# Performance work log

Measured on AMD Instinct MI355X. Metric: run time of the kernel, lower is better.

## Reference

```python
import jax, jax.numpy as jnp
import numpy as np

CUTOFF = 5.0   # radius cutoff r
N_BASIS = 20   # radial Bessel basis size
P = 9          # polynomial cutoff degree
BOX = 40.0     # box edge length (Angstrom) for atom positions
N_ATOMS = 2048


def setup_inputs() -> dict:
    key = jax.random.key(0)
    # atoms uniformly distributed in a cubic box -> realistic sparse radius graph
    pos = jax.random.uniform(key, (N_ATOMS, 3), dtype=jnp.float32) * BOX
    return {"pos": pos}


def reference(pos):
    """EdgeEmbedding.forward (cell=None, batch=None), dense-masked jit form.

    Returns:
      dist_edge: [N, N, n_basis]  envelope(d/r) * bessel(d/r), zero outside radius/diagonal
      dir_edge:  [N, N, 3]        unit displacement vectors, zero outside radius/diagonal
      mask:      [N, N] bool      valid-edge mask (replaces dynamic edge_index)
    """
    r, p, n_basis = CUTOFF, P, N_BASIS
    n = pos.shape[0]
    disp = pos[:, None, :] - pos[None, :, :]          # [N, N, 3], disp[i,j] = pos[i]-pos[j]
    dist = jnp.sqrt(jnp.sum(disp * disp, axis=-1))    # [N, N]
    eye = jnp.eye(n, dtype=bool)
    mask = (dist < r) & (~eye)                        # RadiusGraph: i != j and |d| < r

    safe_dist = jnp.where(mask, dist, 1.0)            # avoid 0-div on diagonal / masked
    dir_edge = jnp.where(mask[..., None], disp / safe_dist[..., None], 0.0)  # ScaledNorm dir
    x = safe_dist / r                                 # ScaledNorm scaled distance

    # PolynomialCutoff: 1 - .5(p+1)(p+2)x^p + p(p+2)x^(p+1) - .5 p(p+1)x^(p+2)
    xp = x ** p
    env = 1.0 - 0.5 * (p + 1) * (p + 2) * xp + p * (p + 2) * xp * x - 0.5 * p * (p + 1) * xp * x * x

    # RadialBesselLayer: sin(k*pi*x)/x for k = 1..n_basis
    freqs = jnp.arange(1, n_basis + 1, dtype=pos.dtype) * jnp.pi  # [n_basis]
    bessel = jnp.sin(freqs * x[..., None]) / x[..., None]         # [N, N, n_basis]

    dist_edge = jnp.where(mask[..., None], env[..., None] * bessel, 0.0)
    return (dist_edge, dir_edge, mask)
```

## Files before the change

### kernel.cpp

```cpp
#include <hip/hip_runtime.h>
#include <math.h>


#define NATOMS 2048
#define NBASIS 20
#define RCUT   5.0f

__global__ __launch_bounds__(256) void edge_scan_kernel(
    const float* __restrict__ pos, float* __restrict__ out)
{
    const int t = threadIdx.x;
    const int i = blockIdx.x >> 3;
    const int j = ((blockIdx.x & 7) << 8) | t;

    const float xi = pos[3 * i + 0], yi = pos[3 * i + 1], zi = pos[3 * i + 2];
    const float xj = pos[3 * j + 0], yj = pos[3 * j + 1], zj = pos[3 * j + 2];
    const float dx = xi - xj, dy = yi - yj, dz = zi - zj;
    float d2;
    {
#pragma clang fp contract(off)
        d2 = (dx * dx + dy * dy) + dz * dz;
    }
    const float dist = sqrtf(d2);
    if (!((dist < RCUT) && (i != j))) return;

    const float x  = dist * (1.0f / RCUT);
    const float x2 = x * x, x4 = x2 * x2, x8 = x4 * x4, x9 = x8 * x;
    const float env = 1.0f - 55.0f * x9 + 99.0f * x9 * x - 45.0f * x9 * x2;
    const float scale = env / x;

    const float theta = 3.14159265358979323846f * x;
    const float s1 = sinf(theta);
    const float twoc = 2.0f * cosf(theta);
    float vals[NBASIS];
    float pm2 = 0.0f, pm1 = s1;
    vals[0] = scale * s1;
#pragma unroll
    for (int k = 1; k < NBASIS; ++k) {
        const float sk = twoc * pm1 - pm2;
        vals[k] = scale * sk;
        pm2 = pm1; pm1 = sk;
    }

    const long long pair = (long long)i * NATOMS + j;
    float4* __restrict__ deq = (float4*)(out + pair * NBASIS);
#pragma unroll
    for (int q = 0; q < 5; ++q)
        deq[q] = make_float4(vals[4 * q + 0], vals[4 * q + 1], vals[4 * q + 2], vals[4 * q + 3]);

    const float inv = 1.0f / dist;
    float* __restrict__ dir = out + (long long)NATOMS * NATOMS * NBASIS + pair * 3;
    dir[0] = dx * inv; dir[1] = dy * inv; dir[2] = dz * inv;
    out[(long long)NATOMS * NATOMS * (NBASIS + 3) + pair] = 1.0f;
}

extern "C" void kernel_launch(void* const* d_in, const int* in_sizes, int n_in,
                              void* d_out, int out_size, void* d_ws, size_t ws_size,
                              hipStream_t stream) {
    const float* pos = (const float*)d_in[0];
    float* out = (float*)d_out;
    hipMemsetAsync(out, 0, (size_t)out_size * sizeof(float), stream);
    edge_scan_kernel<<<dim3(NATOMS * 8), dim3(256), 0, stream>>>(pos, out);
}
```

Measured before the change: 406.3 us.

## Fuse zero-fill into single grid-stride kernel writing every output element once

Drops the separate memset plus sparse scattered writes. One persistent grid-stride kernel now writes every float4 of the basis, direction and mask regions directly, computing zeros for masked pairs. Each output byte is written once and coalesced instead of twice. The cost is recomputing the pair distance per float4 chunk, and doing sin evaluations per chunk rather than once per pair.

```diff
diff --git a/kernel.cpp b/kernel.cpp
--- a/kernel.cpp
+++ b/kernel.cpp
@@ -2,56 +2,117 @@
 #include <math.h>
 
 
-#define NATOMS 2048
-#define NBASIS 20
-#define RCUT   5.0f
+#define NATOMS  2048
+#define NBASIS  20
+#define RCUT    5.0f
+#define NTHREADS (4096 * 256)
 
-__global__ __launch_bounds__(256) void edge_scan_kernel(
+__global__ __launch_bounds__(256) void edge_embed_fused(
     const float* __restrict__ pos, float* __restrict__ out)
 {
-    const int t = threadIdx.x;
-    const int i = blockIdx.x >> 3;
-    const int j = ((blockIdx.x & 7) << 8) | t;
+    const unsigned tid = blockIdx.x * 256u + threadIdx.x;
 
-    const float xi = pos[3 * i + 0], yi = pos[3 * i + 1], zi = pos[3 * i + 2];
-    const float xj = pos[3 * j + 0], yj = pos[3 * j + 1], zj = pos[3 * j + 2];
-    const float dx = xi - xj, dy = yi - yj, dz = zi - zj;
-    float d2;
     {
+        float4* __restrict__ deq = (float4*)out;
+        const unsigned nqA = (unsigned)NATOMS * NATOMS * 5u;
+#pragma unroll 1
+        for (unsigned g = tid; g < nqA; g += NTHREADS) {
+            const unsigned pair = __umulhi(g, 0xCCCCCCCDu) >> 2;
+            const unsigned q    = g - pair * 5u;
+            const unsigned i    = pair >> 11, j = pair & 2047u;
+            const float xi = pos[3*i], yi = pos[3*i+1], zi = pos[3*i+2];
+            const float xj = pos[3*j], yj = pos[3*j+1], zj = pos[3*j+2];
+            const float dx = xi - xj, dy = yi - yj, dz = zi - zj;
+            float d2;
+            {
 #pragma clang fp contract(off)
-        d2 = (dx * dx + dy * dy) + dz * dz;
-    }
-    const float dist = sqrtf(d2);
-    if (!((dist < RCUT) && (i != j))) return;
-
-    const float x  = dist * (1.0f / RCUT);
-    const float x2 = x * x, x4 = x2 * x2, x8 = x4 * x4, x9 = x8 * x;
-    const float env = 1.0f - 55.0f * x9 + 99.0f * x9 * x - 45.0f * x9 * x2;
-    const float scale = env / x;
-
-    const float theta = 3.14159265358979323846f * x;
-    const float s1 = sinf(theta);
-    const float twoc = 2.0f * cosf(theta);
-    float vals[NBASIS];
-    float pm2 = 0.0f, pm1 = s1;
-    vals[0] = scale * s1;
-#pragma unroll
-    for (int k = 1; k < NBASIS; ++k) {
-        const float sk = twoc * pm1 - pm2;
-        vals[k] = scale * sk;
-        pm2 = pm1; pm1 = sk;
+                d2 = (dx * dx + dy * dy) + dz * dz;
+            }
+            const float dist = sqrtf(d2);
+            float4 v = make_float4(0.f, 0.f, 0.f, 0.f);
+            if ((dist < RCUT) && (i != j)) {
+                const float x  = dist * (1.0f / RCUT);
+                const float x2 = x * x, x4 = x2 * x2, x8 = x4 * x4, x9 = x8 * x;
+                const float env = 1.0f - 55.0f * x9 + 99.0f * x9 * x - 45.0f * x9 * x2;
+                const float scale = env / x;
+                const float theta = 3.14159265358979323846f * x;
+                const float k0 = (float)(4u * q + 1u);
+                const float s0 = sinf(k0 * theta);
+                const float s1 = sinf(k0 * theta + theta);
+                const float twoc = 2.0f * cosf(theta);
+                const float s2 = twoc * s1 - s0;
+                const float s3 = twoc * s2 - s1;
+                v = make_float4(scale * s0, scale * s1, scale * s2, scale * s3);
+            }
+            deq[g] = v;
+        }
     }
 
-    const long long pair = (long long)i * NATOMS + j;
-    float4* __restrict__ deq = (float4*)(out + pair * NBASIS);
+    {
+        float4* __restrict__ dirq = (float4*)(out + (size_t)NATOMS * NATOMS * NBASIS);
+        const unsigned nqB = (unsigned)NATOMS * NATOMS * 3u / 4u;
+#pragma unroll 1
+        for (unsigned g = tid; g < nqB; g += NTHREADS) {
+            const unsigned f0 = 4u * g;
+            const unsigned p0 = __umulhi(f0, 0xAAAAAAABu) >> 1;
+            const unsigned c0 = f0 - p0 * 3u;
+            float o[6];
 #pragma unroll
-    for (int q = 0; q < 5; ++q)
-        deq[q] = make_float4(vals[4 * q + 0], vals[4 * q + 1], vals[4 * q + 2], vals[4 * q + 3]);
+            for (int s = 0; s < 2; ++s) {
+                const unsigned p = p0 + (unsigned)s;
+                const unsigned i = (p >> 11) & 2047u, j = p & 2047u;
+                const float dx = pos[3*i]   - pos[3*j];
+                const float dy = pos[3*i+1] - pos[3*j+1];
+                const float dz = pos[3*i+2] - pos[3*j+2];
+                float d2;
+                {
+#pragma clang fp contract(off)
+                    d2 = (dx * dx + dy * dy) + dz * dz;
+                }
+                const float dist = sqrtf(d2);
+                const bool m = (dist < RCUT) && (i != j);
+                const float inv = m ? (1.0f / dist) : 0.0f;
+                o[3*s]   = dx * inv;
+                o[3*s+1] = dy * inv;
+                o[3*s+2] = dz * inv;
+            }
+            float4 v;
+            float* ve = (float*)&v;
+#pragma unroll
+            for (int e = 0; e < 4; ++e) {
+                const unsigned ce = c0 + (unsigned)e;
+                ve[e] = (ce == 0) ? o[0] : (ce == 1) ? o[1] : (ce == 2) ? o[2]
+                       : (ce == 3) ? o[3] : (ce == 4) ? o[4] : o[5];
+            }
+            dirq[g] = v;
+        }
+    }
 
-    const float inv = 1.0f / dist;
-    float* __restrict__ dir = out + (long long)NATOMS * NATOMS * NBASIS + pair * 3;
-    dir[0] = dx * inv; dir[1] = dy * inv; dir[2] = dz * inv;
-    out[(long long)NATOMS * NATOMS * (NBASIS + 3) + pair] = 1.0f;
+    {
+        float4* __restrict__ mq = (float4*)(out + (size_t)NATOMS * NATOMS * (NBASIS + 3));
+        const unsigned nqC = (unsigned)NATOMS * NATOMS / 4u;
+#pragma unroll 1
+        for (unsigned g = tid; g < nqC; g += NTHREADS) {
+            const unsigned p0 = 4u * g;
+            const unsigned i = p0 >> 11, j0 = p0 & 2047u;
+            const float xi = pos[3*i], yi = pos[3*i+1], zi = pos[3*i+2];
+            float4 v;
+            float* ve = (float*)&v;
+#pragma unroll
+            for (int e = 0; e < 4; ++e) {
+                const unsigned j = j0 + (unsigned)e;
+                const float dx = xi - pos[3*j], dy = yi - pos[3*j+1], dz = zi - pos[3*j+2];
+                float d2;
+                {
+#pragma clang fp contract(off)
+                    d2 = (dx * dx + dy * dy) + dz * dz;
+                }
+                const float dist = sqrtf(d2);
+                ve[e] = ((dist < RCUT) && (i != j)) ? 1.0f : 0.0f;
+            }
+            mq[g] = v;
+        }
+    }
 }
 
 extern "C" void kernel_launch(void* const* d_in, const int* in_sizes, int n_in,
@@ -59,6 +120,5 @@
                               hipStream_t stream) {
     const float* pos = (const float*)d_in[0];
     float* out = (float*)d_out;
-    hipMemsetAsync(out, 0, (size_t)out_size * sizeof(float), stream);
-    edge_scan_kernel<<<dim3(NATOMS * 8), dim3(256), 0, stream>>>(pos, out);
+    edge_embed_fused<<<dim3(4096), dim3(256), 0, stream>>>(pos, out);
 }
```

New measurement: 397.1 us. 1.02x faster.
